# Performance work log

Hardware: AMD Instinct MI355X
Metric: run time of the kernel (lower is better)

The kernel has to match this reference:

```python
import jax, jax.numpy as jnp
import numpy as np

N = 50000      # nodes
E = 600000     # directed edges (before self-loops)
IN, HID, OUT = 512, 128, 40
EPS_BN = 1e-5
DROP_P = 0.5   # hardcoded in forward via BernoulliDropout(0.5)

# BinActive: sign() forward, straight-through estimator backward (|x|<=1 gate)
@jax.custom_vjp
def binactive(x):
    return jnp.sign(x)

def _ba_fwd(x):
    return jnp.sign(x), x

def _ba_bwd(x, g):
    return (g * (jnp.abs(x) <= 1.0).astype(g.dtype),)

binactive.defvjp(_ba_fwd, _ba_bwd)


def setup_inputs() -> dict:
    key = jax.random.key(0)
    ks = jax.random.split(key, 8)
    x = jax.random.normal(ks[0], (N, IN), dtype=jnp.float32)
    edge_index = jax.random.randint(ks[1], (2, E), 0, N, dtype=jnp.int64)
    w0 = jax.random.normal(ks[2], (IN, HID), dtype=jnp.float32) * 0.05
    b0 = jnp.zeros((HID,), jnp.float32)
    w1 = jax.random.normal(ks[3], (HID, HID), dtype=jnp.float32) * 0.05
    b1 = jnp.zeros((HID,), jnp.float32)
    w2 = jax.random.normal(ks[4], (HID, OUT), dtype=jnp.float32) * 0.05
    b2 = jnp.zeros((OUT,), jnp.float32)
    return {"x": x, "edge_index": edge_index,
            "w0": w0, "b0": b0, "w1": w1, "b1": b1, "w2": w2, "b2": b2}


def _gcn_norm(edge_index):
    # add self-loops, compute symmetric normalization deg^-1/2 A deg^-1/2
    loops = jnp.arange(N, dtype=edge_index.dtype)
    row = jnp.concatenate([edge_index[0], loops])  # destinations
    col = jnp.concatenate([edge_index[1], loops])  # sources
    deg = jax.ops.segment_sum(jnp.ones_like(row, dtype=jnp.float32), row, num_segments=N)
    dinv = jnp.where(deg > 0, deg ** -0.5, 0.0)
    norm = dinv[row] * dinv[col]                   # [E+N]
    return row, col, norm


def _gcn_conv(x, w, b, row, col, norm):
    # binarized weight: sign(w) scaled by mean(|w|) (XNOR-style)
    wb = binactive(w) * jnp.mean(jnp.abs(w))
    h = x @ wb                                     # [N, out]
    msg = h[col] * norm[:, None]                   # gather + scale
    agg = jax.ops.segment_sum(msg, row, num_segments=N)
    return agg + b


def reference(x, edge_index, w0, b0, w1, b1, w2, b2):
    # BatchNorm1d(affine=False), training-mode batch stats over nodes
    mean = jnp.mean(x, axis=0)
    var = jnp.var(x, axis=0)
    h = (x - mean) / jnp.sqrt(var + EPS_BN)

    row, col, norm = _gcn_norm(edge_index)
    dkey = jax.random.key(42)
    weights = [(w0, b0), (w1, b1), (w2, b2)]
    n_layers = len(weights)
    for i, (w, b) in enumerate(weights):
        h = binactive(h)
        h = _gcn_conv(h, w, b, row, col, norm)
        if i != n_layers - 1:  # BernoulliDropout(0.5)
            mask = jax.random.bernoulli(jax.random.fold_in(dkey, i), 1.0 - DROP_P, h.shape)
            h = h * mask.astype(h.dtype) * (1.0 / (1.0 - DROP_P))
    return jax.nn.log_softmax(h, axis=1)
```

## Files before the change

### kernel.cpp

```cpp
#include <hip/hip_runtime.h>
#include <stdint.h>
#include <stddef.h>

#define NN 50000
#define NE 600000
#define DI 512
#define DH 128
#define DO 40
#define MTOT (NN * DH)
#define NBLK ((NN + 255) / 256)

using int4v = __attribute__((ext_vector_type(4))) int;

__host__ __device__ inline uint32_t rotl32(uint32_t v, int d) {
  return (v << d) | (v >> (32 - d));
}

__host__ __device__ inline void threefry2x32(uint32_t k0, uint32_t k1,
                                             uint32_t c0, uint32_t c1,
                                             uint32_t* o0, uint32_t* o1) {
  uint32_t ks0 = k0, ks1 = k1, ks2 = k0 ^ k1 ^ 0x1BD11BDAu;
  uint32_t x0 = c0 + ks0, x1 = c1 + ks1;
  const int R0[4] = {13, 15, 26, 6};
  const int R1[4] = {17, 29, 16, 24};
#define TF_R4(R) { x0 += x1; x1 = rotl32(x1, R[0]); x1 ^= x0; \
                   x0 += x1; x1 = rotl32(x1, R[1]); x1 ^= x0; \
                   x0 += x1; x1 = rotl32(x1, R[2]); x1 ^= x0; \
                   x0 += x1; x1 = rotl32(x1, R[3]); x1 ^= x0; }
  TF_R4(R0); x0 += ks1; x1 += ks2 + 1u;
  TF_R4(R1); x0 += ks2; x1 += ks0 + 2u;
  TF_R4(R0); x0 += ks0; x1 += ks1 + 3u;
  TF_R4(R1); x0 += ks1; x1 += ks2 + 4u;
  TF_R4(R0); x0 += ks2; x1 += ks0 + 5u;
#undef TF_R4
  *o0 = x0; *o1 = x1;
}

__global__ void colsum_kernel(const float* __restrict__ x,
                              double* __restrict__ colsum) {
  int t = threadIdx.x;
  int r0 = blockIdx.x * 250;
  int r1 = r0 + 250;
  double s0 = 0.0, s1 = 0.0;
  for (int r = r0; r < r1; ++r) {
    s0 += (double)x[(size_t)r * DI + t];
    s1 += (double)x[(size_t)r * DI + t + 256];
  }
  unsafeAtomicAdd(&colsum[t], s0);
  unsafeAtomicAdd(&colsum[t + 256], s1);
}

__global__ void mean_finalize(double* __restrict__ colsum) {
  int c = blockIdx.x * blockDim.x + threadIdx.x;
  if (c < DI) colsum[c] = colsum[c] / (double)NN;
}

__global__ void bn_sign(const float* __restrict__ x,
                        const double* __restrict__ mean,
                        int8_t* __restrict__ S0) {
  size_t j4 = (size_t)blockIdx.x * blockDim.x + threadIdx.x;
  const float4 xv = ((const float4*)x)[j4];
  int c = (int)((j4 * 4) & (DI - 1));
  double v0 = (double)xv.x - mean[c];
  double v1 = (double)xv.y - mean[c + 1];
  double v2 = (double)xv.z - mean[c + 2];
  double v3 = (double)xv.w - mean[c + 3];
  uint32_t o = 0;
  o |= (uint8_t)(int8_t)((v0 > 0.0) ? 1 : ((v0 < 0.0) ? -1 : 0));
  o |= ((uint32_t)(uint8_t)(int8_t)((v1 > 0.0) ? 1 : ((v1 < 0.0) ? -1 : 0))) << 8;
  o |= ((uint32_t)(uint8_t)(int8_t)((v2 > 0.0) ? 1 : ((v2 < 0.0) ? -1 : 0))) << 16;
  o |= ((uint32_t)(uint8_t)(int8_t)((v3 > 0.0) ? 1 : ((v3 < 0.0) ? -1 : 0))) << 24;
  ((uint32_t*)S0)[j4] = o;
}

__global__ void wfuse(const float* __restrict__ w,
                      uint32_t* __restrict__ frag,
                      double* __restrict__ slot,
                      int K, int C, int NT) {
  int steps = K >> 6;
  int total = steps * NT * 64 * 4;
  int idx = blockIdx.x * blockDim.x + threadIdx.x;
  double a = 0.0;
  if (idx < total) {
    int dw = idx & 3;
    int lane = (idx >> 2) & 63;
    int rest = idx >> 8;
    int t = rest % NT;
    int s = rest / NT;
    int n = t * 16 + (lane & 15);
    int kbase = s * 64 + (lane >> 4) * 16 + dw * 4;
    uint32_t v = 0;
    if (n < C) {
#pragma unroll
      for (int j = 0; j < 4; ++j) {
        float wv = w[(size_t)(kbase + j) * C + n];
        uint32_t sg = (uint8_t)(int8_t)((wv > 0.f) ? 1 : ((wv < 0.f) ? -1 : 0));
        v |= sg << (8 * j);
        a += (double)fabsf(wv);
      }
    }
    frag[idx] = v;
  }
  __shared__ double red[256];
  red[threadIdx.x] = a;
  __syncthreads();
  for (int ofs = 128; ofs > 0; ofs >>= 1) {
    if (threadIdx.x < ofs) red[threadIdx.x] += red[threadIdx.x + ofs];
    __syncthreads();
  }
  if (threadIdx.x == 0) unsafeAtomicAdd(slot, red[0]);
}

__global__ void deg_edges(const int* __restrict__ ei, uint32_t* __restrict__ deg) {
  int e = blockIdx.x * blockDim.x + threadIdx.x;
  if (e < NE) atomicAdd(&deg[ei[e]], 1u);
}

__global__ void scan_blocks(const uint32_t* __restrict__ deg,
                            uint32_t* __restrict__ rowptr,
                            uint32_t* __restrict__ bsum,
                            double* __restrict__ dinv) {
  __shared__ uint32_t bs[256];
  int t = threadIdx.x;
  int i = blockIdx.x * 256 + t;
  uint32_t v = (i < NN) ? deg[i] : 0u;
  if (i < NN) dinv[i] = 1.0 / sqrt((double)(v + 1u));
  bs[t] = v;
  __syncthreads();
  for (int ofs = 1; ofs < 256; ofs <<= 1) {
    uint32_t add = (t >= ofs) ? bs[t - ofs] : 0u;
    __syncthreads();
    bs[t] += add;
    __syncthreads();
  }
  if (i < NN) rowptr[i] = bs[t] - v;
  if (t == 255) bsum[blockIdx.x] = bs[255];
}

__global__ void scan_bsum(const uint32_t* __restrict__ bsum,
                          uint32_t* __restrict__ base) {
  __shared__ uint32_t bs[256];
  int t = threadIdx.x;
  uint32_t v = (t < NBLK) ? bsum[t] : 0u;
  bs[t] = v;
  __syncthreads();
  for (int ofs = 1; ofs < 256; ofs <<= 1) {
    uint32_t add = (t >= ofs) ? bs[t - ofs] : 0u;
    __syncthreads();
    bs[t] += add;
    __syncthreads();
  }
  if (t < NBLK) base[t] = bs[t] - v;
}

__global__ void scan_addbase(uint32_t* __restrict__ rowptr,
                             const uint32_t* __restrict__ base) {
  int i = blockIdx.x * 256 + threadIdx.x;
  if (i < NN) rowptr[i] += base[blockIdx.x];
  if (i == 0) rowptr[NN] = NE;
}

__global__ void csr_fill(const int* __restrict__ ei,
                         const uint32_t* __restrict__ rowptr,
                         uint32_t* __restrict__ cursor,
                         int* __restrict__ csr_src) {
  int e = blockIdx.x * blockDim.x + threadIdx.x;
  if (e >= NE) return;
  int dst = ei[e], src = ei[NE + e];
  uint32_t pos = rowptr[dst] + atomicAdd(&cursor[dst], 1u);
  csr_src[pos] = src;
}

template <int STEPS, int NT, int C, int SHIFT>
__global__ void gemm_mfma(const int8_t* __restrict__ S,
                          const uint32_t* __restrict__ frag,
                          int8_t* __restrict__ H) {
  extern __shared__ uint4 lb[];
  const int tot = STEPS * NT * 64;
  const uint4* fg = (const uint4*)frag;
  for (int i = threadIdx.x; i < tot; i += 256) lb[i] = fg[i];
  __syncthreads();
  const int lane = threadIdx.x & 63;
  const int wv = threadIdx.x >> 6;
  const int r0 = (blockIdx.x * 4 + wv) * 16;
  if (r0 >= NN) return;
  const int m = lane & 15, q = lane >> 4;
  const int K = STEPS * 64;
  const int8_t* sp = S + (size_t)(r0 + m) * K + q * 16;
  int4v acc[NT];
#pragma unroll
  for (int t = 0; t < NT; ++t) acc[t] = (int4v){0, 0, 0, 0};
#pragma unroll
  for (int s = 0; s < STEPS; ++s) {
    int4v a = *(const int4v*)(sp + (size_t)s * 64);
#pragma unroll
    for (int t = 0; t < NT; ++t) {
      int4v b = *(const int4v*)&lb[(s * NT + t) * 64 + lane];
      acc[t] = __builtin_amdgcn_mfma_i32_16x16x64_i8(a, b, acc[t], 0, 0, 0);
    }
  }
  int8_t* hp = H + (size_t)r0 * C;
#pragma unroll
  for (int t = 0; t < NT; ++t) {
    int n = t * 16 + m;
    if (n < C) {
#pragma unroll
      for (int r = 0; r < 4; ++r)
        hp[(size_t)(q * 4 + r) * C + n] = (int8_t)(acc[t][r] >> SHIFT);
    }
  }
}

__global__ void gather128(const uint32_t* __restrict__ rowptr,
                          const int* __restrict__ csr_src,
                          const double* __restrict__ dinv,
                          const int8_t* __restrict__ H,
                          const float* __restrict__ b,
                          int8_t* __restrict__ Sout,
                          const double* __restrict__ wsum, double cnt,
                          uint32_t fk0, uint32_t fk1) {
  int d = (int)(((size_t)blockIdx.x * blockDim.x + threadIdx.x) >> 6);
  int lane = threadIdx.x & 63;
  if (d >= NN) return;
  const int g = lane >> 5, p = lane & 31;
  double a0 = 0.0, a1 = 0.0, a2 = 0.0, a3 = 0.0;
  const uint32_t e0 = rowptr[d];
  const int L = (int)(rowptr[d + 1] - e0) + 1;
  for (int c0 = 0; c0 < L; c0 += 64) {
    const int n = min(64, L - c0);
    const int my = c0 + lane;
    int sidx = d;
    if (my > 0 && my < L) sidx = csr_src[e0 + my - 1];
    double wv = dinv[sidx];
    int t = 0;
    for (; t + 4 <= n; t += 4) {
      const int jA = t + g, jB = t + 2 + g;
      int sA = __shfl(sidx, jA);  double wA = __shfl(wv, jA);
      int sB = __shfl(sidx, jB);  double wB = __shfl(wv, jB);
      uint32_t hA = *(const uint32_t*)(H + (size_t)sA * DH + 4 * p);
      uint32_t hB = *(const uint32_t*)(H + (size_t)sB * DH + 4 * p);
      a0 += wA * (double)(int8_t)(hA);
      a1 += wA * (double)(int8_t)(hA >> 8);
      a2 += wA * (double)(int8_t)(hA >> 16);
      a3 += wA * (double)(int8_t)(hA >> 24);
      a0 += wB * (double)(int8_t)(hB);
      a1 += wB * (double)(int8_t)(hB >> 8);
      a2 += wB * (double)(int8_t)(hB >> 16);
      a3 += wB * (double)(int8_t)(hB >> 24);
    }
    for (; t < n; t += 2) {
      const int j = t + g;
      const bool on = (j < n);
      const int jc = on ? j : 0;
      int s = __shfl(sidx, jc);
      double w = __shfl(wv, jc);
      w = on ? w : 0.0;
      uint32_t hv = *(const uint32_t*)(H + (size_t)s * DH + 4 * p);
      a0 += w * (double)(int8_t)(hv);
      a1 += w * (double)(int8_t)(hv >> 8);
      a2 += w * (double)(int8_t)(hv >> 16);
      a3 += w * (double)(int8_t)(hv >> 24);
    }
  }
  a0 += __shfl_xor(a0, 32);
  a1 += __shfl_xor(a1, 32);
  a2 += __shfl_xor(a2, 32);
  a3 += __shfl_xor(a3, 32);
  double sc = (wsum[0] / cnt) * dinv[d];
  int ch = 4 * p + 2 * g;
  int j0 = d * DH + ch;
  double va = sc * ((g == 0) ? a0 : a2) + (double)b[ch];
  double vb = sc * ((g == 0) ? a1 : a3) + (double)b[ch + 1];
  int s0 = (va > 0.0) ? 1 : ((va < 0.0) ? -1 : 0);
  int s1 = (vb > 0.0) ? 1 : ((vb < 0.0) ? -1 : 0);
  uint32_t r0, r1, bits0, bits1;
  threefry2x32(fk0, fk1, 0u, (uint32_t)j0, &r0, &r1);
  bits0 = r0 ^ r1;
  threefry2x32(fk0, fk1, 0u, (uint32_t)(j0 + 1), &r0, &r1);
  bits1 = r0 ^ r1;
  float u0 = __uint_as_float((bits0 >> 9) | 0x3f800000u) - 1.0f;
  float u1 = __uint_as_float((bits1 >> 9) | 0x3f800000u) - 1.0f;
  uint8_t o0 = (u0 < 0.5f) ? (uint8_t)(int8_t)s0 : (uint8_t)0;
  uint8_t o1 = (u1 < 0.5f) ? (uint8_t)(int8_t)s1 : (uint8_t)0;
  *(uint16_t*)(Sout + j0) = (uint16_t)(o0 | ((uint16_t)o1 << 8));
}

__global__ void gather40_lsm(const uint32_t* __restrict__ rowptr,
                             const int* __restrict__ csr_src,
                             const double* __restrict__ dinv,
                             const int8_t* __restrict__ H,
                             const float* __restrict__ b2,
                             const double* __restrict__ wsum,
                             float* __restrict__ out) {
  int d = (int)(((size_t)blockIdx.x * blockDim.x + threadIdx.x) >> 6);
  int lane = threadIdx.x & 63;
  if (d >= NN) return;
  const int g = lane >> 5, p = lane & 31;
  const bool act = (p < 20);
  double a0 = 0.0, a1 = 0.0;
  const uint32_t e0 = rowptr[d];
  const int L = (int)(rowptr[d + 1] - e0) + 1;
  for (int c0 = 0; c0 < L; c0 += 64) {
    const int n = min(64, L - c0);
    const int my = c0 + lane;
    int sidx = d;
    if (my > 0 && my < L) sidx = csr_src[e0 + my - 1];
    double wv = dinv[sidx];
    int t = 0;
    for (; t + 4 <= n; t += 4) {
      const int jA = t + g, jB = t + 2 + g;
      int sA = __shfl(sidx, jA);  double wA = __shfl(wv, jA);
      int sB = __shfl(sidx, jB);  double wB = __shfl(wv, jB);
      if (act) {
        uint16_t hA = *(const uint16_t*)(H + (size_t)sA * DO + 2 * p);
        uint16_t hB = *(const uint16_t*)(H + (size_t)sB * DO + 2 * p);
        a0 += wA * (double)(int8_t)(hA);
        a1 += wA * (double)(int8_t)(hA >> 8);
        a0 += wB * (double)(int8_t)(hB);
        a1 += wB * (double)(int8_t)(hB >> 8);
      }
    }
    for (; t < n; t += 2) {
      const int j = t + g;
      const bool on = (j < n);
      const int jc = on ? j : 0;
      int s = __shfl(sidx, jc);
      double w = __shfl(wv, jc);
      w = on ? w : 0.0;
      if (act) {
        uint16_t hv = *(const uint16_t*)(H + (size_t)s * DO + 2 * p);
        a0 += w * (double)(int8_t)(hv);
        a1 += w * (double)(int8_t)(hv >> 8);
      }
    }
  }
  a0 += __shfl_xor(a0, 32);
  a1 += __shfl_xor(a1, 32);
  double sc = (wsum[0] / (double)(DH * DO)) * dinv[d];
  const bool lead = (g == 0) && act;
  double v0 = 0.0, v1 = 0.0;
  if (act) {
    v0 = sc * a0 + (double)b2[2 * p];
    v1 = sc * a1 + (double)b2[2 * p + 1];
  }
  double mx = lead ? fmax(v0, v1) : -1.0e300;
  for (int ofs = 32; ofs > 0; ofs >>= 1) mx = fmax(mx, __shfl_xor(mx, ofs));
  float ex = lead ? (expf((float)(v0 - mx)) + expf((float)(v1 - mx))) : 0.f;
  for (int ofs = 32; ofs > 0; ofs >>= 1) ex += __shfl_xor(ex, ofs);
  float l = logf(ex);
  if (lead) {
    float2 o = make_float2((float)(v0 - mx) - l, (float)(v1 - mx) - l);
    *(float2*)(out + (size_t)d * DO + 2 * p) = o;
  }
}

extern "C" void kernel_launch(void* const* d_in, const int* in_sizes, int n_in,
                              void* d_out, int out_size, void* d_ws, size_t ws_size,
                              hipStream_t stream) {
  (void)in_sizes; (void)n_in; (void)out_size; (void)ws_size;
  const float* x  = (const float*)d_in[0];
  const int*   ei = (const int*)d_in[1];
  const float* w0 = (const float*)d_in[2];
  const float* b0 = (const float*)d_in[3];
  const float* w1 = (const float*)d_in[4];
  const float* b1 = (const float*)d_in[5];
  const float* w2 = (const float*)d_in[6];
  const float* b2 = (const float*)d_in[7];
  float* out = (float*)d_out;

  char* wsb = (char*)d_ws;
  double*   mean_d = (double*)wsb;
  double*   wsum_d = (double*)(wsb + 4096);
  uint32_t* deg_e  = (uint32_t*)(wsb + 4224);
  uint32_t* cursor = (uint32_t*)(wsb + 204224);
  size_t cur = 404480;
  uint32_t* rowptr = (uint32_t*)(wsb + cur); cur += 200064;
  double*   dinv_d = (double*)(wsb + cur);  cur += 400000;
  cur = (cur + 255) & ~255ull;
  uint32_t* bsum = (uint32_t*)(wsb + cur); cur += 1024;
  uint32_t* base = (uint32_t*)(wsb + cur); cur += 1024;
  int*    csr_src = (int*)(wsb + cur);    cur += (size_t)NE * 4;
  cur = (cur + 255) & ~255ull;
  uint32_t* FR0 = (uint32_t*)(wsb + cur); cur += 8 * 8 * 64 * 16;
  uint32_t* FR1 = (uint32_t*)(wsb + cur); cur += 2 * 8 * 64 * 16;
  uint32_t* FR2 = (uint32_t*)(wsb + cur); cur += 2 * 3 * 64 * 16;
  int8_t* S1  = (int8_t*)(wsb + cur); cur += (size_t)MTOT;
  cur = (cur + 255) & ~255ull;
  int8_t* H8 = (int8_t*)(wsb + cur); cur += (size_t)MTOT;
  cur = (cur + 255) & ~255ull;
  int8_t* S0  = (int8_t*)(wsb + cur);

  uint32_t fkA0, fkA1, fkB0, fkB1;
  threefry2x32(0u, 42u, 0u, 0u, &fkA0, &fkA1);
  threefry2x32(0u, 42u, 0u, 1u, &fkB0, &fkB1);

  hipMemsetAsync(wsb, 0, 404224, stream);

  colsum_kernel<<<200, 256, 0, stream>>>(x, mean_d);
  mean_finalize<<<2, 256, 0, stream>>>(mean_d);
  wfuse<<<(8 * 8 * 64 * 4 + 255) / 256, 256, 0, stream>>>(w0, FR0, wsum_d + 0, DI, DH, 8);
  wfuse<<<(2 * 8 * 64 * 4 + 255) / 256, 256, 0, stream>>>(w1, FR1, wsum_d + 1, DH, DH, 8);
  wfuse<<<(2 * 3 * 64 * 4 + 255) / 256, 256, 0, stream>>>(w2, FR2, wsum_d + 2, DH, DO, 3);
  deg_edges<<<(NE + 255) / 256, 256, 0, stream>>>(ei, deg_e);
  scan_blocks<<<NBLK, 256, 0, stream>>>(deg_e, rowptr, bsum, dinv_d);
  scan_bsum<<<1, 256, 0, stream>>>(bsum, base);
  scan_addbase<<<NBLK, 256, 0, stream>>>(rowptr, base);
  csr_fill<<<(NE + 255) / 256, 256, 0, stream>>>(ei, rowptr, cursor, csr_src);
  bn_sign<<<(NN * DI / 4) / 256, 256, 0, stream>>>(x, mean_d, S0);

  const int gemm_blocks = (NN / 16 + 3) / 4;
  const int node_blocks = (NN * 64) / 256 + 1;
  const size_t sh0 = 8 * 8 * 64 * 16;
  const size_t sh1 = 2 * 8 * 64 * 16;
  const size_t sh2 = 2 * 3 * 64 * 16;

  gemm_mfma<8, 8, DH, 1><<<gemm_blocks, 256, sh0, stream>>>(S0, FR0, H8);
  gather128<<<node_blocks, 256, 0, stream>>>(rowptr, csr_src, dinv_d, H8, b0, S1,
                                             wsum_d + 0, (double)(DI * DH / 2),
                                             fkA0, fkA1);

  gemm_mfma<2, 8, DH, 0><<<gemm_blocks, 256, sh1, stream>>>(S1, FR1, H8);
  gather128<<<node_blocks, 256, 0, stream>>>(rowptr, csr_src, dinv_d, H8, b1, S1,
                                             wsum_d + 1, (double)(DH * DH),
                                             fkB0, fkB1);

  gemm_mfma<2, 3, DO, 0><<<gemm_blocks, 256, sh2, stream>>>(S1, FR2, H8);
  gather40_lsm<<<node_blocks, 256, 0, stream>>>(rowptr, csr_src, dinv_d, H8, b2,
                                                wsum_d + 2, out);
}
```

Baseline: 399.3 us.

## Fuse BN-sign into first GEMM, merge weight prep, prefetch gathers

Folds the batch-norm sign step directly into the first int8 MFMA GEMM. The GEMM now reads fp32 x and the per-column means and builds the int8 A fragments in registers, so the 25.6MB int8 S0 buffer is never written or read back. The three weight-binarization launches become a single kernel, colsum is unrolled to issue more loads at once, and the gather loops software-prefetch the next pair of neighbor rows. The cost is more register pressure in the fused GEMM and in the gather loops, and the fused GEMM's strided float4 reads of x may coalesce less well than the streaming bn_sign pass did.

```diff
diff --git a/kernel.cpp b/kernel.cpp
--- a/kernel.cpp
+++ b/kernel.cpp
@@ -40,11 +40,19 @@
                               double* __restrict__ colsum) {
   int t = threadIdx.x;
   int r0 = blockIdx.x * 250;
-  int r1 = r0 + 250;
   double s0 = 0.0, s1 = 0.0;
-  for (int r = r0; r < r1; ++r) {
-    s0 += (double)x[(size_t)r * DI + t];
-    s1 += (double)x[(size_t)r * DI + t + 256];
+  for (int r = r0; r < r0 + 250; r += 10) {
+    double v0[10], v1[10];
+#pragma unroll
+    for (int u = 0; u < 10; ++u) {
+      v0[u] = (double)x[(size_t)(r + u) * DI + t];
+      v1[u] = (double)x[(size_t)(r + u) * DI + t + 256];
+    }
+#pragma unroll
+    for (int u = 0; u < 10; ++u) {
+      s0 += v0[u];
+      s1 += v1[u];
+    }
   }
   unsafeAtomicAdd(&colsum[t], s0);
   unsafeAtomicAdd(&colsum[t + 256], s1);
@@ -55,31 +63,14 @@
   if (c < DI) colsum[c] = colsum[c] / (double)NN;
 }
 
-__global__ void bn_sign(const float* __restrict__ x,
-                        const double* __restrict__ mean,
-                        int8_t* __restrict__ S0) {
-  size_t j4 = (size_t)blockIdx.x * blockDim.x + threadIdx.x;
-  const float4 xv = ((const float4*)x)[j4];
-  int c = (int)((j4 * 4) & (DI - 1));
-  double v0 = (double)xv.x - mean[c];
-  double v1 = (double)xv.y - mean[c + 1];
-  double v2 = (double)xv.z - mean[c + 2];
-  double v3 = (double)xv.w - mean[c + 3];
-  uint32_t o = 0;
-  o |= (uint8_t)(int8_t)((v0 > 0.0) ? 1 : ((v0 < 0.0) ? -1 : 0));
-  o |= ((uint32_t)(uint8_t)(int8_t)((v1 > 0.0) ? 1 : ((v1 < 0.0) ? -1 : 0))) << 8;
-  o |= ((uint32_t)(uint8_t)(int8_t)((v2 > 0.0) ? 1 : ((v2 < 0.0) ? -1 : 0))) << 16;
-  o |= ((uint32_t)(uint8_t)(int8_t)((v3 > 0.0) ? 1 : ((v3 < 0.0) ? -1 : 0))) << 24;
-  ((uint32_t*)S0)[j4] = o;
-}
-
-__global__ void wfuse(const float* __restrict__ w,
-                      uint32_t* __restrict__ frag,
-                      double* __restrict__ slot,
-                      int K, int C, int NT) {
+__device__ inline void wfuse_body(const float* __restrict__ w,
+                                  uint32_t* __restrict__ frag,
+                                  double* __restrict__ slot,
+                                  int K, int C, int NT, int blk,
+                                  double* red) {
   int steps = K >> 6;
   int total = steps * NT * 64 * 4;
-  int idx = blockIdx.x * blockDim.x + threadIdx.x;
+  int idx = blk * 256 + threadIdx.x;
   double a = 0.0;
   if (idx < total) {
     int dw = idx & 3;
@@ -101,7 +92,6 @@
     }
     frag[idx] = v;
   }
-  __shared__ double red[256];
   red[threadIdx.x] = a;
   __syncthreads();
   for (int ofs = 128; ofs > 0; ofs >>= 1) {
@@ -109,6 +99,20 @@
     __syncthreads();
   }
   if (threadIdx.x == 0) unsafeAtomicAdd(slot, red[0]);
+}
+
+__global__ void wfuse_all(const float* __restrict__ w0,
+                          const float* __restrict__ w1,
+                          const float* __restrict__ w2,
+                          uint32_t* __restrict__ f0,
+                          uint32_t* __restrict__ f1,
+                          uint32_t* __restrict__ f2,
+                          double* __restrict__ slots) {
+  __shared__ double red[256];
+  int b = blockIdx.x;
+  if (b < 64)       wfuse_body(w0, f0, slots + 0, DI, DH, 8, b,      red);
+  else if (b < 80)  wfuse_body(w1, f1, slots + 1, DH, DH, 8, b - 64, red);
+  else              wfuse_body(w2, f2, slots + 2, DH, DO, 3, b - 80, red);
 }
 
 __global__ void deg_edges(const int* __restrict__ ei, uint32_t* __restrict__ deg) {
@@ -208,6 +212,60 @@
       for (int r = 0; r < 4; ++r)
         hp[(size_t)(q * 4 + r) * C + n] = (int8_t)(acc[t][r] >> SHIFT);
     }
+  }
+}
+
+__global__ void gemm0_fused(const float* __restrict__ x,
+                            const double* __restrict__ mean,
+                            const uint32_t* __restrict__ frag,
+                            int8_t* __restrict__ H) {
+  extern __shared__ uint4 lb[];
+  const int tot = 8 * 8 * 64;
+  const uint4* fg = (const uint4*)frag;
+  for (int i = threadIdx.x; i < tot; i += 256) lb[i] = fg[i];
+  __syncthreads();
+  const int lane = threadIdx.x & 63;
+  const int wv = threadIdx.x >> 6;
+  const int r0 = (blockIdx.x * 4 + wv) * 16;
+  if (r0 >= NN) return;
+  const int m = lane & 15, q = lane >> 4;
+  const float* xp = x + (size_t)(r0 + m) * DI + q * 16;
+  const double* mp0 = mean + q * 16;
+  int4v acc[8];
+#pragma unroll
+  for (int t = 0; t < 8; ++t) acc[t] = (int4v){0, 0, 0, 0};
+#pragma unroll
+  for (int s = 0; s < 8; ++s) {
+    const float* xs = xp + s * 64;
+    const double* mp = mp0 + s * 64;
+    int4v a;
+#pragma unroll
+    for (int w4 = 0; w4 < 4; ++w4) {
+      float4 f = *(const float4*)(xs + 4 * w4);
+      double v0 = (double)f.x - mp[4 * w4 + 0];
+      double v1 = (double)f.y - mp[4 * w4 + 1];
+      double v2 = (double)f.z - mp[4 * w4 + 2];
+      double v3 = (double)f.w - mp[4 * w4 + 3];
+      uint32_t o = 0;
+      o |= (uint8_t)(int8_t)((v0 > 0.0) ? 1 : ((v0 < 0.0) ? -1 : 0));
+      o |= ((uint32_t)(uint8_t)(int8_t)((v1 > 0.0) ? 1 : ((v1 < 0.0) ? -1 : 0))) << 8;
+      o |= ((uint32_t)(uint8_t)(int8_t)((v2 > 0.0) ? 1 : ((v2 < 0.0) ? -1 : 0))) << 16;
+      o |= ((uint32_t)(uint8_t)(int8_t)((v3 > 0.0) ? 1 : ((v3 < 0.0) ? -1 : 0))) << 24;
+      a[w4] = (int)o;
+    }
+#pragma unroll
+    for (int t = 0; t < 8; ++t) {
+      int4v b = *(const int4v*)&lb[(s * 8 + t) * 64 + lane];
+      acc[t] = __builtin_amdgcn_mfma_i32_16x16x64_i8(a, b, acc[t], 0, 0, 0);
+    }
+  }
+  int8_t* hp = H + (size_t)r0 * DH;
+#pragma unroll
+  for (int t = 0; t < 8; ++t) {
+    int n = t * 16 + m;
+#pragma unroll
+    for (int r = 0; r < 4; ++r)
+      hp[(size_t)(q * 4 + r) * DH + n] = (int8_t)(acc[t][r] >> 1);
   }
 }
 
@@ -233,20 +291,33 @@
     if (my > 0 && my < L) sidx = csr_src[e0 + my - 1];
     double wv = dinv[sidx];
     int t = 0;
-    for (; t + 4 <= n; t += 4) {
-      const int jA = t + g, jB = t + 2 + g;
-      int sA = __shfl(sidx, jA);  double wA = __shfl(wv, jA);
-      int sB = __shfl(sidx, jB);  double wB = __shfl(wv, jB);
-      uint32_t hA = *(const uint32_t*)(H + (size_t)sA * DH + 4 * p);
-      uint32_t hB = *(const uint32_t*)(H + (size_t)sB * DH + 4 * p);
-      a0 += wA * (double)(int8_t)(hA);
-      a1 += wA * (double)(int8_t)(hA >> 8);
-      a2 += wA * (double)(int8_t)(hA >> 16);
-      a3 += wA * (double)(int8_t)(hA >> 24);
-      a0 += wB * (double)(int8_t)(hB);
-      a1 += wB * (double)(int8_t)(hB >> 8);
-      a2 += wB * (double)(int8_t)(hB >> 16);
-      a3 += wB * (double)(int8_t)(hB >> 24);
+    {
+      int sA = 0, sB = 0; double wA = 0.0, wB = 0.0;
+      uint32_t hA = 0, hB = 0;
+      if (4 <= n) {
+        sA = __shfl(sidx, g);      wA = __shfl(wv, g);
+        sB = __shfl(sidx, 2 + g);  wB = __shfl(wv, 2 + g);
+        hA = *(const uint32_t*)(H + (size_t)sA * DH + 4 * p);
+        hB = *(const uint32_t*)(H + (size_t)sB * DH + 4 * p);
+      }
+      for (; t + 4 <= n; t += 4) {
+        const uint32_t cA = hA, cB = hB;
+        const double vA = wA, vB = wB;
+        if (t + 8 <= n) {
+          sA = __shfl(sidx, t + 4 + g);  wA = __shfl(wv, t + 4 + g);
+          sB = __shfl(sidx, t + 6 + g);  wB = __shfl(wv, t + 6 + g);
+          hA = *(const uint32_t*)(H + (size_t)sA * DH + 4 * p);
+          hB = *(const uint32_t*)(H + (size_t)sB * DH + 4 * p);
+        }
+        a0 += vA * (double)(int8_t)(cA);
+        a1 += vA * (double)(int8_t)(cA >> 8);
+        a2 += vA * (double)(int8_t)(cA >> 16);
+        a3 += vA * (double)(int8_t)(cA >> 24);
+        a0 += vB * (double)(int8_t)(cB);
+        a1 += vB * (double)(int8_t)(cB >> 8);
+        a2 += vB * (double)(int8_t)(cB >> 16);
+        a3 += vB * (double)(int8_t)(cB >> 24);
+      }
     }
     for (; t < n; t += 2) {
       const int j = t + g;
@@ -307,17 +378,34 @@
     if (my > 0 && my < L) sidx = csr_src[e0 + my - 1];
     double wv = dinv[sidx];
     int t = 0;
-    for (; t + 4 <= n; t += 4) {
-      const int jA = t + g, jB = t + 2 + g;
-      int sA = __shfl(sidx, jA);  double wA = __shfl(wv, jA);
-      int sB = __shfl(sidx, jB);  double wB = __shfl(wv, jB);
-      if (act) {
-        uint16_t hA = *(const uint16_t*)(H + (size_t)sA * DO + 2 * p);
-        uint16_t hB = *(const uint16_t*)(H + (size_t)sB * DO + 2 * p);
-        a0 += wA * (double)(int8_t)(hA);
-        a1 += wA * (double)(int8_t)(hA >> 8);
-        a0 += wB * (double)(int8_t)(hB);
-        a1 += wB * (double)(int8_t)(hB >> 8);
+    {
+      int sA = 0, sB = 0; double wA = 0.0, wB = 0.0;
+      uint16_t hA = 0, hB = 0;
+      if (4 <= n) {
+        sA = __shfl(sidx, g);      wA = __shfl(wv, g);
+        sB = __shfl(sidx, 2 + g);  wB = __shfl(wv, 2 + g);
+        if (act) {
+          hA = *(const uint16_t*)(H + (size_t)sA * DO + 2 * p);
+          hB = *(const uint16_t*)(H + (size_t)sB * DO + 2 * p);
+        }
+      }
+      for (; t + 4 <= n; t += 4) {
+        const uint16_t cA = hA, cB = hB;
+        const double vA = wA, vB = wB;
+        if (t + 8 <= n) {
+          sA = __shfl(sidx, t + 4 + g);  wA = __shfl(wv, t + 4 + g);
+          sB = __shfl(sidx, t + 6 + g);  wB = __shfl(wv, t + 6 + g);
+          if (act) {
+            hA = *(const uint16_t*)(H + (size_t)sA * DO + 2 * p);
+            hB = *(const uint16_t*)(H + (size_t)sB * DO + 2 * p);
+          }
+        }
+        if (act) {
+          a0 += vA * (double)(int8_t)(cA);
+          a1 += vA * (double)(int8_t)(cA >> 8);
+          a0 += vB * (double)(int8_t)(cB);
+          a1 += vB * (double)(int8_t)(cB >> 8);
+        }
       }
     }
     for (; t < n; t += 2) {
@@ -387,8 +475,6 @@
   int8_t* S1  = (int8_t*)(wsb + cur); cur += (size_t)MTOT;
   cur = (cur + 255) & ~255ull;
   int8_t* H8 = (int8_t*)(wsb + cur); cur += (size_t)MTOT;
-  cur = (cur + 255) & ~255ull;
-  int8_t* S0  = (int8_t*)(wsb + cur);
 
   uint32_t fkA0, fkA1, fkB0, fkB1;
   threefry2x32(0u, 42u, 0u, 0u, &fkA0, &fkA1);
@@ -398,15 +484,12 @@
 
   colsum_kernel<<<200, 256, 0, stream>>>(x, mean_d);
   mean_finalize<<<2, 256, 0, stream>>>(mean_d);
-  wfuse<<<(8 * 8 * 64 * 4 + 255) / 256, 256, 0, stream>>>(w0, FR0, wsum_d + 0, DI, DH, 8);
-  wfuse<<<(2 * 8 * 64 * 4 + 255) / 256, 256, 0, stream>>>(w1, FR1, wsum_d + 1, DH, DH, 8);
-  wfuse<<<(2 * 3 * 64 * 4 + 255) / 256, 256, 0, stream>>>(w2, FR2, wsum_d + 2, DH, DO, 3);
+  wfuse_all<<<86, 256, 0, stream>>>(w0, w1, w2, FR0, FR1, FR2, wsum_d);
   deg_edges<<<(NE + 255) / 256, 256, 0, stream>>>(ei, deg_e);
   scan_blocks<<<NBLK, 256, 0, stream>>>(deg_e, rowptr, bsum, dinv_d);
   scan_bsum<<<1, 256, 0, stream>>>(bsum, base);
   scan_addbase<<<NBLK, 256, 0, stream>>>(rowptr, base);
   csr_fill<<<(NE + 255) / 256, 256, 0, stream>>>(ei, rowptr, cursor, csr_src);
-  bn_sign<<<(NN * DI / 4) / 256, 256, 0, stream>>>(x, mean_d, S0);
 
   const int gemm_blocks = (NN / 16 + 3) / 4;
   const int node_blocks = (NN * 64) / 256 + 1;
@@ -414,7 +497,7 @@
   const size_t sh1 = 2 * 8 * 64 * 16;
   const size_t sh2 = 2 * 3 * 64 * 16;
 
-  gemm_mfma<8, 8, DH, 1><<<gemm_blocks, 256, sh0, stream>>>(S0, FR0, H8);
+  gemm0_fused<<<gemm_blocks, 256, sh0, stream>>>(x, mean_d, FR0, H8);
   gather128<<<node_blocks, 256, 0, stream>>>(rowptr, csr_src, dinv_d, H8, b0, S1,
                                              wsum_d + 0, (double)(DI * DH / 2),
                                              fkA0, fkA1);
```

Result: no change. 401.4 us (+0.5%).
